# Optimization experiments

Measured on AMD Instinct MI355X. Metric: run time of the kernel, lower is better.

## Reference

```python
import jax, jax.numpy as jnp
import numpy as np
from jax import lax

B, T, H, W, C = 1, 8, 32, 32, 512


def _rmsnorm(x, gamma):
    # x / (||x||_2 + 1e-8) * sqrt(C) * gamma  (matches FlaxHunyuanVideo15RMSNorm)
    n = x / (jnp.linalg.norm(x, axis=-1, keepdims=True) + 1e-8)
    return n * (x.shape[-1] ** 0.5) * gamma


def _conv3d(x, w, b):
    # x: [B,T,H,W,Cin], w: [kt,kh,kw,Cin,Cout] (DHWIO), VALID padding
    y = lax.conv_general_dilated(x, w, (1, 1, 1), 'VALID',
                                 dimension_numbers=('NDHWC', 'DHWIO', 'NDHWC'))
    return y + b


def _causal_conv3d(x, w, b):
    # replicate pad: time (2,0) causal, spatial (1,1) each side, then valid 3x3x3 conv
    xp = jnp.pad(x, [(0, 0), (2, 0), (1, 1), (1, 1), (0, 0)], mode='edge')
    return _conv3d(xp, w, b)


def _conv1x1(x, w, b):
    # w: [1,1,1,Cin,Cout]
    return jnp.einsum('bthwc,cd->bthwd', x, w[0, 0, 0]) + b


def _resnet(x, g1, w1, b1, g2, w2, b2):
    h = jax.nn.silu(_rmsnorm(x, g1))
    h = _causal_conv3d(h, w1, b1)
    h = jax.nn.silu(_rmsnorm(h, g2))
    h = _causal_conv3d(h, w2, b2)
    return h + x


def _attn(x, g, qw, qb, kw, kb, vw, vb, pw, pb):
    identity = x
    xn = _rmsnorm(x, g)
    b, t, h, w, c = xn.shape
    n_hw = h * w
    s = t * n_hw
    q = _conv1x1(xn, qw, qb).reshape(b, s, c)
    k = _conv1x1(xn, kw, kb).reshape(b, s, c)
    v = _conv1x1(xn, vw, vb).reshape(b, s, c)
    # block-causal frame mask: query at frame f attends to keys with frame <= f
    fid = jnp.arange(s) // n_hw
    mask = jnp.where(fid[None, :] <= fid[:, None], 0.0, -jnp.inf).astype(q.dtype)
    scale = 1.0 / jnp.sqrt(jnp.asarray(c, q.dtype))
    scores = jnp.einsum('bqc,bkc->bqk', q, k) * scale + mask  # [B,S,S]
    attn = jax.nn.softmax(scores, axis=-1)
    o = jnp.einsum('bqk,bkc->bqc', attn, v).reshape(b, t, h, w, c)
    o = _conv1x1(o, pw, pb)
    return o + identity


def _forward(x, r1_g1, r1_w1, r1_b1, r1_g2, r1_w2, r1_b2,
             at_g, q_w, q_b, k_w, k_b, v_w, v_b, p_w, p_b,
             r2_g1, r2_w1, r2_b1, r2_g2, r2_w2, r2_b2):
    h = _resnet(x, r1_g1, r1_w1, r1_b1, r1_g2, r1_w2, r1_b2)
    h = _attn(h, at_g, q_w, q_b, k_w, k_b, v_w, v_b, p_w, p_b)
    h = _resnet(h, r2_g1, r2_w1, r2_b1, r2_g2, r2_w2, r2_b2)
    return h


def setup_inputs() -> dict:
    key = jax.random.key(0)
    ks = jax.random.split(key, 10)
    w3 = lambda k: jax.random.normal(k, (3, 3, 3, C, C), jnp.float32) * 0.02
    w1 = lambda k: jax.random.normal(k, (1, 1, 1, C, C), jnp.float32) * 0.02
    zc = jnp.zeros((C,), jnp.float32)
    oc = jnp.ones((C,), jnp.float32)
    return dict(
        x=jax.random.normal(ks[0], (B, T, H, W, C), jnp.float32),
        r1_g1=oc, r1_w1=w3(ks[1]), r1_b1=zc,
        r1_g2=oc, r1_w2=w3(ks[2]), r1_b2=zc,
        at_g=oc,
        q_w=w1(ks[3]), q_b=zc,
        k_w=w1(ks[4]), k_b=zc,
        v_w=w1(ks[5]), v_b=zc,
        p_w=w1(ks[6]), p_b=zc,
        r2_g1=oc, r2_w1=w3(ks[7]), r2_b1=zc,
        r2_g2=oc, r2_w2=w3(ks[8]), r2_b2=zc,
    )


def reference(x, r1_g1, r1_w1, r1_b1, r1_g2, r1_w2, r1_b2,
              at_g, q_w, q_b, k_w, k_b, v_w, v_b, p_w, p_b,
              r2_g1, r2_w1, r2_b1, r2_g2, r2_w2, r2_b2):
    return _forward(x, r1_g1, r1_w1, r1_b1, r1_g2, r1_w2, r1_b2,
                    at_g, q_w, q_b, k_w, k_b, v_w, v_b, p_w, p_b,
                    r2_g1, r2_w1, r2_b1, r2_g2, r2_w2, r2_b2)
```

## Files before the change

### kernel.cpp

```cpp
#include <hip/hip_runtime.h>
#include <cstdint>
#include <cstddef>

typedef __attribute__((ext_vector_type(4))) float floatx4;
typedef __attribute__((ext_vector_type(8))) short short8;

__device__ __forceinline__ short f2bf(float x) {
  union { float f; unsigned u; } c; c.f = x;
  unsigned r = (c.u + 0x7FFFu + ((c.u >> 16) & 1u)) >> 16;
  return (short)r;
}

__device__ __forceinline__ float bf2f(short x) {
  union { unsigned u; float f; } c; c.u = ((unsigned)(unsigned short)x) << 16;
  return c.f;
}

__device__ __forceinline__ floatx4 mfma16(short8 a, short8 b, floatx4 c) {
  return __builtin_amdgcn_mfma_f32_16x16x32_bf16(a, b, c, 0, 0, 0);
}

template <typename T>
__device__ __forceinline__ void gl_lds16(const T* g, T* l) {
  __builtin_amdgcn_global_load_lds(
      (__attribute__((address_space(1))) void*)g,
      (__attribute__((address_space(3))) void*)l, 16, 0, 0);
}

#define MEMFENCE asm volatile("" ::: "memory")
#define WAITV8 asm volatile("s_waitcnt vmcnt(8)" ::: "memory")

template <bool PAD, bool SILU>
__global__ __launch_bounds__(256) void norm_kernel(const float* __restrict__ src,
                                                   const float* __restrict__ gamma,
                                                   short* __restrict__ dst) {
  const int tid = threadIdx.x;
  const int wv = tid >> 6, lane = tid & 63;
  const int id = blockIdx.x * 4 + wv;
  int srow;
  if (PAD) {
    int tp = id / 1156, rem = id - tp * 1156;
    int hp = rem / 34, wp = rem - hp * 34;
    int t = tp - 2; t = t < 0 ? 0 : t;
    int h = hp - 1; h = h < 0 ? 0 : (h > 31 ? 31 : h);
    int w = wp - 1; w = w < 0 ? 0 : (w > 31 ? 31 : w);
    srow = (t << 10) + (h << 5) + w;
  } else {
    srow = id;
  }
  const float* sp = src + (size_t)srow * 512 + lane * 8;
  float4 v0 = *(const float4*)sp;
  float4 v1 = *(const float4*)(sp + 4);
  float a[8] = {v0.x, v0.y, v0.z, v0.w, v1.x, v1.y, v1.z, v1.w};
  float ss = 0.f;
#pragma unroll
  for (int i = 0; i < 8; ++i) ss += a[i] * a[i];
#pragma unroll
  for (int off = 32; off > 0; off >>= 1) ss += __shfl_xor(ss, off);
  const float scale = 22.627416997969522f / (sqrtf(ss) + 1e-8f);
  const float* gp = gamma + lane * 8;
  float4 g0 = *(const float4*)gp;
  float4 g1 = *(const float4*)(gp + 4);
  float g[8] = {g0.x, g0.y, g0.z, g0.w, g1.x, g1.y, g1.z, g1.w};
  short8 ov;
#pragma unroll
  for (int i = 0; i < 8; ++i) {
    float y = a[i] * scale * g[i];
    if (SILU) y = y / (1.f + __expf(-y));
    ov[i] = f2bf(y);
  }
  *(short8*)(dst + (size_t)id * 512 + lane * 8) = ov;
}

template <int NP>
__global__ __launch_bounds__(256) void combine_norm(const float* __restrict__ P0,
                                                    const float* __restrict__ P1,
                                                    const float* __restrict__ P2,
                                                    const float* __restrict__ bias,
                                                    const float* __restrict__ gamma,
                                                    short* __restrict__ dst) {
  const int tid = threadIdx.x;
  const int wv = tid >> 6, lane = tid & 63;
  const int id = blockIdx.x * 4 + wv;
  int tp = id / 1156, rem = id - tp * 1156;
  int hp = rem / 34, wp = rem - hp * 34;
  int t = tp - 2; t = t < 0 ? 0 : t;
  int h = hp - 1; h = h < 0 ? 0 : (h > 31 ? 31 : h);
  int w = wp - 1; w = w < 0 ? 0 : (w > 31 ? 31 : w);
  const size_t base = (size_t)((t << 10) + (h << 5) + w) * 512 + lane * 8;
  float a[8];
  {
    float4 a0 = *(const float4*)(P0 + base), a1 = *(const float4*)(P0 + base + 4);
    float4 b0 = *(const float4*)(P1 + base), b1 = *(const float4*)(P1 + base + 4);
    float4 z0 = *(const float4*)(bias + lane * 8), z1 = *(const float4*)(bias + lane * 8 + 4);
    a[0] = a0.x + b0.x + z0.x; a[1] = a0.y + b0.y + z0.y;
    a[2] = a0.z + b0.z + z0.z; a[3] = a0.w + b0.w + z0.w;
    a[4] = a1.x + b1.x + z1.x; a[5] = a1.y + b1.y + z1.y;
    a[6] = a1.z + b1.z + z1.z; a[7] = a1.w + b1.w + z1.w;
    if (NP == 3) {
      float4 c0 = *(const float4*)(P2 + base), c1 = *(const float4*)(P2 + base + 4);
      a[0] += c0.x; a[1] += c0.y; a[2] += c0.z; a[3] += c0.w;
      a[4] += c1.x; a[5] += c1.y; a[6] += c1.z; a[7] += c1.w;
    }
  }
  float ss = 0.f;
#pragma unroll
  for (int i = 0; i < 8; ++i) ss += a[i] * a[i];
#pragma unroll
  for (int off = 32; off > 0; off >>= 1) ss += __shfl_xor(ss, off);
  const float scale = 22.627416997969522f / (sqrtf(ss) + 1e-8f);
  float4 g0 = *(const float4*)(gamma + lane * 8), g1 = *(const float4*)(gamma + lane * 8 + 4);
  float g[8] = {g0.x, g0.y, g0.z, g0.w, g1.x, g1.y, g1.z, g1.w};
  short8 ov;
#pragma unroll
  for (int i = 0; i < 8; ++i) {
    float y = a[i] * scale * g[i];
    y = y / (1.f + __expf(-y));
    ov[i] = f2bf(y);
  }
  *(short8*)(dst + (size_t)id * 512 + lane * 8) = ov;
}

__global__ __launch_bounds__(256) void transpose_w(const float* __restrict__ src,
                                                   short* __restrict__ dst, int R, int C) {
  __shared__ float t[32][33];
  const int tx = threadIdx.x & 31, ty = threadIdx.x >> 5;
  const int r0 = (int)blockIdx.x << 5, c0 = (int)blockIdx.y << 5;
#pragma unroll
  for (int i = 0; i < 4; ++i)
    t[ty + i * 8][tx] = src[(size_t)(r0 + ty + i * 8) * C + c0 + tx];
  __syncthreads();
#pragma unroll
  for (int i = 0; i < 4; ++i)
    dst[(size_t)(c0 + ty + i * 8) * R + r0 + tx] = f2bf(t[tx][ty + i * 8]);
}

template <int NP>
__global__ __launch_bounds__(256) void conv_gemm_sp(const short* __restrict__ Xp,
                                                    const short* __restrict__ WT,
                                                    float* __restrict__ P0,
                                                    float* __restrict__ P1,
                                                    float* __restrict__ P2) {
  __shared__ __attribute__((aligned(16))) short Alds[2][4096];
  __shared__ __attribute__((aligned(16))) short Blds[2][4096];
  const int tid = threadIdx.x;
  const int wv = tid >> 6, lane = tid & 63;
  const int m0 = (int)blockIdx.x << 7, n0 = (int)blockIdx.y << 7;
  const int z = blockIdx.z;
  float* __restrict__ dst = (NP == 3) ? (z == 0 ? P0 : (z == 1 ? P1 : P2))
                                      : (z ? P1 : P0);

  const int swz = (((lane & 3) ^ ((lane >> 3) & 3)) << 3);
  int aoff[2], boff[2];
#pragma unroll
  for (int j = 0; j < 2; ++j) {
    const int chunk = wv * 2 + j;
    const int m = m0 + chunk * 16 + (lane >> 2);
    const int t = m >> 10, h = (m >> 5) & 31, w = m & 31;
    aoff[j] = (t * 1156 + h * 34 + w) * 512 + swz;
    const int n = n0 + chunk * 16 + (lane >> 2);
    boff[j] = n * 13824 + swz;
  }
  const int wm = (wv & 1) << 6, wn = (wv >> 1) << 6;
  floatx4 acc[4][4];
#pragma unroll
  for (int i = 0; i < 4; ++i)
#pragma unroll
    for (int j = 0; j < 4; ++j) acc[i][j] = 0.f;

  const int la = (lane & 15) * 32 + ((((lane >> 4) ^ ((lane >> 1) & 3))) << 3);
  const int span = 432 / NP;
  const int k0 = z * span, k1 = k0 + span;

  auto stage = [&](int kk, int buf) {
    const int tap = kk >> 4;
    const int cin0 = (kk & 15) << 5;
    const int dt = tap / 9;
    const int r9 = tap - dt * 9;
    const int dh = r9 / 3;
    const int dw = r9 - dh * 3;
    const int tapoff = (dt * 1156 + dh * 34 + dw) * 512 + cin0;
#pragma unroll
    for (int j = 0; j < 2; ++j) {
      const int chunk = wv * 2 + j;
      gl_lds16(Xp + aoff[j] + tapoff, &Alds[buf][chunk * 512]);
      gl_lds16(WT + boff[j] + (kk << 5), &Blds[buf][chunk * 512]);
    }
  };

  stage(k0, 0);
  for (int kk = k0; kk < k1; ++kk) {
    const int cur = (kk - k0) & 1;
    __syncthreads();
    if (kk + 1 < k1) stage(kk + 1, cur ^ 1);
    short8 af[4], bf[4];
#pragma unroll
    for (int i = 0; i < 4; ++i) af[i] = *(const short8*)&Alds[cur][(wm + i * 16) * 32 + la];
#pragma unroll
    for (int j = 0; j < 4; ++j) bf[j] = *(const short8*)&Blds[cur][(wn + j * 16) * 32 + la];
#pragma unroll
    for (int i = 0; i < 4; ++i)
#pragma unroll
      for (int j = 0; j < 4; ++j) acc[i][j] = mfma16(af[i], bf[j], acc[i][j]);
  }

  const int rbase = m0 + wm + (lane >> 4) * 4;
#pragma unroll
  for (int i = 0; i < 4; ++i) {
    const int row = rbase + i * 16;
#pragma unroll
    for (int j = 0; j < 4; ++j) {
      const int col = n0 + wn + j * 16 + (lane & 15);
#pragma unroll
      for (int r = 0; r < 4; ++r)
        dst[(size_t)(row + r) * 512 + col] = acc[i][j][r];
    }
  }
}

template <int NP, bool HAS_RES>
__global__ __launch_bounds__(256) void conv_combine(const float* __restrict__ P0,
                                                    const float* __restrict__ P1,
                                                    const float* __restrict__ P2,
                                                    const float* __restrict__ bias,
                                                    const float* __restrict__ res,
                                                    float* __restrict__ out) {
  const size_t i = ((size_t)blockIdx.x * 256 + threadIdx.x) * 4;
  float4 a = *(const float4*)(P0 + i);
  float4 b = *(const float4*)(P1 + i);
  float4 bz = *(const float4*)(bias + (int)(i & 511));
  float4 r;
  r.x = a.x + b.x + bz.x;
  r.y = a.y + b.y + bz.y;
  r.z = a.z + b.z + bz.z;
  r.w = a.w + b.w + bz.w;
  if (NP == 3) {
    float4 c = *(const float4*)(P2 + i);
    r.x += c.x; r.y += c.y; r.z += c.z; r.w += c.w;
  }
  if (HAS_RES) {
    float4 rs = *(const float4*)(res + i);
    r.x += rs.x; r.y += rs.y; r.z += rs.z; r.w += rs.w;
  }
  *(float4*)(out + i) = r;
}

template <int EPI>
__global__ __launch_bounds__(256) void gemm_bt(const short* __restrict__ A,
                                               const short* __restrict__ BT, int kdim,
                                               const float* __restrict__ b0,
                                               const float* __restrict__ b1,
                                               const float* __restrict__ b2,
                                               short* __restrict__ o0,
                                               short* __restrict__ o1,
                                               short* __restrict__ o2,
                                               float* oF, const float* res) {
  __shared__ __attribute__((aligned(16))) short Alds[2][4096];
  __shared__ __attribute__((aligned(16))) short Blds[2][4096];
  const int tid = threadIdx.x;
  const int wv = tid >> 6, lane = tid & 63;
  const int m0 = (int)blockIdx.x << 7, n0 = (int)blockIdx.y << 7;
  const int swz = (((lane & 3) ^ ((lane >> 3) & 3)) << 3);
  int aoff[2], boff[2];
#pragma unroll
  for (int j = 0; j < 2; ++j) {
    const int chunk = wv * 2 + j;
    aoff[j] = (m0 + chunk * 16 + (lane >> 2)) * kdim + swz;
    boff[j] = (n0 + chunk * 16 + (lane >> 2)) * kdim + swz;
  }
  const int wm = (wv & 1) << 6, wn = (wv >> 1) << 6;
  floatx4 acc[4][4];
#pragma unroll
  for (int i = 0; i < 4; ++i)
#pragma unroll
    for (int j = 0; j < 4; ++j) acc[i][j] = 0.f;
  const int la = (lane & 15) * 32 + ((((lane >> 4) ^ ((lane >> 1) & 3))) << 3);
  const int kiters = kdim >> 5;

  auto stage = [&](int kk, int buf) {
#pragma unroll
    for (int j = 0; j < 2; ++j) {
      const int chunk = wv * 2 + j;
      gl_lds16(A + aoff[j] + (kk << 5), &Alds[buf][chunk * 512]);
      gl_lds16(BT + boff[j] + (kk << 5), &Blds[buf][chunk * 512]);
    }
  };

  stage(0, 0);
  for (int kk = 0; kk < kiters; ++kk) {
    const int cur = kk & 1;
    __syncthreads();
    if (kk + 1 < kiters) stage(kk + 1, cur ^ 1);
    short8 af[4], bf[4];
#pragma unroll
    for (int i = 0; i < 4; ++i) af[i] = *(const short8*)&Alds[cur][(wm + i * 16) * 32 + la];
#pragma unroll
    for (int j = 0; j < 4; ++j) bf[j] = *(const short8*)&Blds[cur][(wn + j * 16) * 32 + la];
#pragma unroll
    for (int i = 0; i < 4; ++i)
#pragma unroll
      for (int j = 0; j < 4; ++j) acc[i][j] = mfma16(af[i], bf[j], acc[i][j]);
  }

  const int rbase = m0 + wm + (lane >> 4) * 4;
#pragma unroll
  for (int i = 0; i < 4; ++i) {
    const int row = rbase + i * 16;
#pragma unroll
    for (int j = 0; j < 4; ++j) {
      const int col = n0 + wn + j * 16 + (lane & 15);
      if (EPI == 0) {
        const int sel = col >> 9;
        const int c = col & 511;
        const float* bp = sel == 0 ? b0 : (sel == 1 ? b1 : b2);
        const float bz = bp[c];
#pragma unroll
        for (int r = 0; r < 4; ++r) {
          const int rr = row + r;
          const short v = f2bf(acc[i][j][r] + bz);
          if (sel == 0) {
            o0[(size_t)rr * 512 + c] = v;
          } else if (sel == 1) {
            o1[(size_t)(rr >> 5) * 16384 + ((c >> 5) << 10) + (((c >> 3) & 3) << 8) +
               ((rr & 31) << 3) + (c & 7)] = v;
          } else {
            o2[(size_t)(rr >> 5) * 16384 + (((rr >> 3) & 3) << 12) + (c << 3) + (rr & 7)] = v;
          }
        }
      } else {
        const float bz = b0[col];
#pragma unroll
        for (int r = 0; r < 4; ++r) {
          const size_t idx = (size_t)(row + r) * 512 + col;
          oF[idx] = acc[i][j][r] + bz + res[idx];
        }
      }
    }
  }
}

__global__ __launch_bounds__(256, 2) void attn_partial(const short* __restrict__ Q,
                                                       const short* __restrict__ Ksw,
                                                       const short* __restrict__ Vsw,
                                                       short* __restrict__ OpA,
                                                       short* __restrict__ OpB,
                                                       float* __restrict__ Lp) {
  __shared__ __attribute__((aligned(16))) short Klds[16384];
  __shared__ __attribute__((aligned(16))) short Vlds[16384];
  __shared__ __attribute__((aligned(16))) short Plds[4][512];
  const int tid = threadIdx.x;
  const int wv = tid >> 6, lane = tid & 63;
  const int cl = lane & 15, quad = lane >> 4;
  const int bid = (int)blockIdx.x;
  const int x8 = bid & 7, jj = bid >> 3;
  int y, qb;
  if (jj < 64) {
    y = x8 + ((jj >> 4) << 3);
    qb = jj & 15;
  } else {
    const int L = x8 * 8 + (jj - 64);
    y = 32 + (L >> 4);
    qb = L & 15;
  }
  int f = 0;
  while ((f + 1) * (f + 2) / 2 <= y) ++f;
  const int chunk = y - f * (f + 1) / 2;
  const int pidx = y * 16 + qb;
  const int q0 = (f << 10) + (qb << 6);

  short8 qf[16];
  {
    const short* qp = Q + (size_t)(q0 + wv * 16 + cl) * 512 + quad * 8;
#pragma unroll
    for (int kc = 0; kc < 16; ++kc) qf[kc] = *(const short8*)(qp + kc * 32);
  }
  floatx4 o[32];
#pragma unroll
  for (int i = 0; i < 32; ++i) o[i] = 0.f;
  float lr[4] = {0.f, 0.f, 0.f, 0.f};
  const float c1 = 0.063758716f;
  const short* klb = Klds + quad * 256 + cl * 8;
  const short* vlb = Vlds + quad * 4096 + cl * 8;
  const int swr = ((cl >> 1) & 3) << 3;

  auto stageK = [&](int kt) {
    const size_t tb = (size_t)((chunk << 5) + kt) * 16384;
#pragma unroll
    for (int j = 0; j < 8; ++j) {
      const int row = (j * 4 + wv) << 9;
      gl_lds16(Ksw + tb + row + lane * 8, &Klds[row]);
    }
  };
  auto stageV = [&](int kt) {
    const size_t tb = (size_t)((chunk << 5) + kt) * 16384;
#pragma unroll
    for (int j = 0; j < 8; ++j) {
      const int row = (j * 4 + wv) << 9;
      gl_lds16(Vsw + tb + row + lane * 8, &Vlds[row]);
    }
  };

  stageK(0);
  stageV(0);

  for (int kt = 0; kt < 32; ++kt) {
    WAITV8;
    __builtin_amdgcn_s_barrier();
    MEMFENCE;

    floatx4 s0 = 0.f, s1 = 0.f;
    __builtin_amdgcn_s_setprio(1);
#pragma unroll
    for (int kc = 0; kc < 16; ++kc) {
      short8 k0 = *(const short8*)(klb + kc * 1024);
      short8 k1 = *(const short8*)(klb + kc * 1024 + 128);
      s0 = mfma16(qf[kc], k0, s0);
      s1 = mfma16(qf[kc], k1, s1);
    }
    __builtin_amdgcn_s_setprio(0);

    MEMFENCE;
    __builtin_amdgcn_s_barrier();
    MEMFENCE;
    if (kt + 1 < 32) stageK(kt + 1);

#pragma unroll
    for (int r = 0; r < 4; ++r) {
      const float p0 = exp2f(s0[r] * c1), p1 = exp2f(s1[r] * c1);
      lr[r] += p0 + p1;
      const int qlr = quad * 4 + r;
      const int sw = ((qlr >> 1) & 3) << 3;
      const int oi = qlr * 32 + (cl ^ sw);
      Plds[wv][oi] = f2bf(p0);
      Plds[wv][oi ^ 16] = f2bf(p1);
    }

    WAITV8;
    __builtin_amdgcn_s_barrier();
    MEMFENCE;

    const short8 pf = *(const short8*)&Plds[wv][cl * 32 + ((quad << 3) ^ swr)];
    __builtin_amdgcn_s_setprio(1);
#pragma unroll
    for (int cn = 0; cn < 32; ++cn) {
      const short8 vf = *(const short8*)(vlb + cn * 128);
      o[cn] = mfma16(pf, vf, o[cn]);
    }
    __builtin_amdgcn_s_setprio(0);

    MEMFENCE;
    __builtin_amdgcn_s_barrier();
    MEMFENCE;
    if (kt + 1 < 32) stageV(kt + 1);
  }

#pragma unroll
  for (int r = 0; r < 4; ++r) {
    float v = lr[r];
    v += __shfl_xor(v, 1);
    v += __shfl_xor(v, 2);
    v += __shfl_xor(v, 4);
    v += __shfl_xor(v, 8);
    lr[r] = v;
  }

  short* base = pidx < 216 ? OpA + (size_t)pidx * 32768 : OpB + (size_t)(pidx - 216) * 32768;
  const int lrow0 = wv * 16 + quad * 4;
#pragma unroll
  for (int cn = 0; cn < 32; ++cn) {
    const int col = cn * 16 + cl;
#pragma unroll
    for (int r = 0; r < 4; ++r)
      base[(size_t)(lrow0 + r) * 512 + col] = f2bf(o[cn][r]);
  }
  if (cl == 0) {
#pragma unroll
    for (int r = 0; r < 4; ++r) Lp[pidx * 64 + lrow0 + r] = lr[r];
  }
}

__global__ __launch_bounds__(256) void attn_combine(const short* __restrict__ OpA,
                                                    const short* __restrict__ OpB,
                                                    const float* __restrict__ Lp,
                                                    short* __restrict__ O) {
  const int tid = threadIdx.x;
  const int wv = tid >> 6, lane = tid & 63;
  const int row = (int)blockIdx.x * 4 + wv;
  const int f = row >> 10, n = f + 1;
  const int qb = (row >> 6) & 15, lrow = row & 63;
  const int tri = f * (f + 1) / 2;
  float den = 0.f, acc[8];
#pragma unroll
  for (int i = 0; i < 8; ++i) acc[i] = 0.f;
#pragma unroll
  for (int ch = 0; ch < 8; ++ch) {
    if (ch < n) {
      const int pidx = (tri + ch) * 16 + qb;
      den += Lp[pidx * 64 + lrow];
      const short* b = pidx < 216 ? OpA + (size_t)pidx * 32768 : OpB + (size_t)(pidx - 216) * 32768;
      const short8 v = *(const short8*)(b + (size_t)lrow * 512 + lane * 8);
#pragma unroll
      for (int i = 0; i < 8; ++i) acc[i] += bf2f(v[i]);
    }
  }
  const float inv = 1.f / den;
  short8 ov;
#pragma unroll
  for (int i = 0; i < 8; ++i) ov[i] = f2bf(acc[i] * inv);
  *(short8*)(O + (size_t)row * 512 + lane * 8) = ov;
}

extern "C" void kernel_launch(void* const* d_in, const int* in_sizes, int n_in,
                              void* d_out, int out_size, void* d_ws, size_t ws_size,
                              hipStream_t stream) {
  const float* x     = (const float*)d_in[0];
  const float* r1_g1 = (const float*)d_in[1];
  const float* r1_w1 = (const float*)d_in[2];
  const float* r1_b1 = (const float*)d_in[3];
  const float* r1_g2 = (const float*)d_in[4];
  const float* r1_w2 = (const float*)d_in[5];
  const float* r1_b2 = (const float*)d_in[6];
  const float* at_g  = (const float*)d_in[7];
  const float* q_w   = (const float*)d_in[8];
  const float* q_b   = (const float*)d_in[9];
  const float* k_w   = (const float*)d_in[10];
  const float* k_b   = (const float*)d_in[11];
  const float* v_w   = (const float*)d_in[12];
  const float* v_b   = (const float*)d_in[13];
  const float* p_w   = (const float*)d_in[14];
  const float* p_b   = (const float*)d_in[15];
  const float* r2_g1 = (const float*)d_in[16];
  const float* r2_w1 = (const float*)d_in[17];
  const float* r2_b1 = (const float*)d_in[18];
  const float* r2_g2 = (const float*)d_in[19];
  const float* r2_w2 = (const float*)d_in[20];
  const float* r2_b2 = (const float*)d_in[21];
  float* out = (float*)d_out;

  char* ws = (char*)d_ws;
  size_t off = 0;
  auto alloc = [&](size_t bytes) -> void* {
    void* p = ws + off;
    off = (off + bytes + 255) & ~(size_t)255;
    return p;
  };
  short* wT    = (short*)alloc(27ull * 512 * 512 * 2);
  short* wqkvT = (short*)alloc(1536ull * 512 * 2);
  short* pwT   = (short*)alloc(512ull * 512 * 2);
  short* Xp    = (short*)alloc(10ull * 34 * 34 * 512 * 2);
  float* Y     = (float*)alloc(8192ull * 512 * 4);
  float* hA    = (float*)alloc(8192ull * 512 * 4);
  short* xn    = (short*)alloc(8192ull * 512 * 2);
  short* Qb    = (short*)alloc(8192ull * 512 * 2);
  short* Ksw   = (short*)alloc(8192ull * 512 * 2);
  short* Vsw   = (short*)alloc(8192ull * 512 * 2);
  float* Lp    = (float*)alloc(576ull * 64 * 4);
  (void)ws_size; (void)in_sizes; (void)n_in; (void)out_size;

  short* OpA = wT;
  short* OpB = Xp;
  float* P0  = (float*)xn;
  float* P1  = (float*)Ksw;
  float* P2  = Y;

  const dim3 b256(256);
  const dim3 convg3(64, 4, 3);
  const dim3 convg2(64, 4, 2);

  transpose_w<<<dim3(432, 16), b256, 0, stream>>>(r1_w1, wT, 13824, 512);
  norm_kernel<true, true><<<2890, b256, 0, stream>>>(x, r1_g1, Xp);
  conv_gemm_sp<3><<<convg3, b256, 0, stream>>>(Xp, wT, P0, P1, P2);
  transpose_w<<<dim3(432, 16), b256, 0, stream>>>(r1_w2, wT, 13824, 512);
  combine_norm<3><<<2890, b256, 0, stream>>>(P0, P1, P2, r1_b1, r1_g2, Xp);
  conv_gemm_sp<3><<<convg3, b256, 0, stream>>>(Xp, wT, P0, P1, P2);
  conv_combine<3, true><<<4096, b256, 0, stream>>>(P0, P1, P2, r1_b2, x, hA);

  norm_kernel<false, false><<<2048, b256, 0, stream>>>(hA, at_g, xn);
  transpose_w<<<dim3(16, 16), b256, 0, stream>>>(q_w, wqkvT, 512, 512);
  transpose_w<<<dim3(16, 16), b256, 0, stream>>>(k_w, wqkvT + 512 * 512, 512, 512);
  transpose_w<<<dim3(16, 16), b256, 0, stream>>>(v_w, wqkvT + 1024 * 512, 512, 512);
  transpose_w<<<dim3(16, 16), b256, 0, stream>>>(p_w, pwT, 512, 512);
  gemm_bt<0><<<dim3(64, 12), b256, 0, stream>>>(xn, wqkvT, 512, q_b, k_b, v_b,
                                                Qb, Ksw, Vsw, nullptr, nullptr);
  attn_partial<<<576, b256, 0, stream>>>(Qb, Ksw, Vsw, OpA, OpB, Lp);
  attn_combine<<<2048, b256, 0, stream>>>(OpA, OpB, Lp, xn);
  gemm_bt<1><<<dim3(64, 4), b256, 0, stream>>>(xn, pwT, 512, p_b, nullptr, nullptr,
                                               nullptr, nullptr, nullptr, hA, hA);

  transpose_w<<<dim3(432, 16), b256, 0, stream>>>(r2_w1, wT, 13824, 512);
  norm_kernel<true, true><<<2890, b256, 0, stream>>>(hA, r2_g1, Xp);
  conv_gemm_sp<2><<<convg2, b256, 0, stream>>>(Xp, wT, P0, P1, P2);
  transpose_w<<<dim3(432, 16), b256, 0, stream>>>(r2_w2, wT, 13824, 512);
  combine_norm<2><<<2890, b256, 0, stream>>>(P0, P1, P2, r2_b1, r2_g2, Xp);
  conv_gemm_sp<2><<<convg2, b256, 0, stream>>>(Xp, wT, P0, P1, P2);
  conv_combine<2, true><<<4096, b256, 0, stream>>>(P0, P1, P2, r2_b2, hA, out);
}
```

Before: 1.039 ms.

## Replace conv GEMM with 256x256-tile 8-wave kernel and uniform 4-way split-K

The causal conv implicit GEMM moves from 128x128 tiles with 4 waves and 3/2-way split-K to 256x256 tiles with 8 waves, 64-wide K steps and a fixed 4-way split-K. Global-to-LDS loads for the next stage are interleaved across four sub-phases with explicit vmcnt waits, barriers and setprio around the MFMA bursts. This aims to raise data reuse per LDS byte and overlap loads with compute. In exchange it needs much more LDS per block, fewer blocks, and an extra partial buffer (aliased to the output) to be summed in the combine kernels.

```diff
diff --git a/kernel.cpp b/kernel.cpp
--- a/kernel.cpp
+++ b/kernel.cpp
@@ -29,6 +29,8 @@
 
 #define MEMFENCE asm volatile("" ::: "memory")
 #define WAITV8 asm volatile("s_waitcnt vmcnt(8)" ::: "memory")
+#define WAITV2 asm volatile("s_waitcnt vmcnt(2)" ::: "memory")
+#define WAITV0 asm volatile("s_waitcnt vmcnt(0)" ::: "memory")
 
 template <bool PAD, bool SILU>
 __global__ __launch_bounds__(256) void norm_kernel(const float* __restrict__ src,
@@ -72,10 +74,10 @@
   *(short8*)(dst + (size_t)id * 512 + lane * 8) = ov;
 }
 
-template <int NP>
 __global__ __launch_bounds__(256) void combine_norm(const float* __restrict__ P0,
                                                     const float* __restrict__ P1,
                                                     const float* __restrict__ P2,
+                                                    const float* __restrict__ P3,
                                                     const float* __restrict__ bias,
                                                     const float* __restrict__ gamma,
                                                     short* __restrict__ dst) {
@@ -92,16 +94,17 @@
   {
     float4 a0 = *(const float4*)(P0 + base), a1 = *(const float4*)(P0 + base + 4);
     float4 b0 = *(const float4*)(P1 + base), b1 = *(const float4*)(P1 + base + 4);
+    float4 c0 = *(const float4*)(P2 + base), c1 = *(const float4*)(P2 + base + 4);
+    float4 d0 = *(const float4*)(P3 + base), d1 = *(const float4*)(P3 + base + 4);
     float4 z0 = *(const float4*)(bias + lane * 8), z1 = *(const float4*)(bias + lane * 8 + 4);
-    a[0] = a0.x + b0.x + z0.x; a[1] = a0.y + b0.y + z0.y;
-    a[2] = a0.z + b0.z + z0.z; a[3] = a0.w + b0.w + z0.w;
-    a[4] = a1.x + b1.x + z1.x; a[5] = a1.y + b1.y + z1.y;
-    a[6] = a1.z + b1.z + z1.z; a[7] = a1.w + b1.w + z1.w;
-    if (NP == 3) {
-      float4 c0 = *(const float4*)(P2 + base), c1 = *(const float4*)(P2 + base + 4);
-      a[0] += c0.x; a[1] += c0.y; a[2] += c0.z; a[3] += c0.w;
-      a[4] += c1.x; a[5] += c1.y; a[6] += c1.z; a[7] += c1.w;
-    }
+    a[0] = a0.x + b0.x + c0.x + d0.x + z0.x;
+    a[1] = a0.y + b0.y + c0.y + d0.y + z0.y;
+    a[2] = a0.z + b0.z + c0.z + d0.z + z0.z;
+    a[3] = a0.w + b0.w + c0.w + d0.w + z0.w;
+    a[4] = a1.x + b1.x + c1.x + d1.x + z1.x;
+    a[5] = a1.y + b1.y + c1.y + d1.y + z1.y;
+    a[6] = a1.z + b1.z + c1.z + d1.z + z1.z;
+    a[7] = a1.w + b1.w + c1.w + d1.w + z1.w;
   }
   float ss = 0.f;
 #pragma unroll
@@ -135,109 +138,163 @@
     dst[(size_t)(c0 + ty + i * 8) * R + r0 + tx] = f2bf(t[tx][ty + i * 8]);
 }
 
-template <int NP>
-__global__ __launch_bounds__(256) void conv_gemm_sp(const short* __restrict__ Xp,
-                                                    const short* __restrict__ WT,
-                                                    float* __restrict__ P0,
-                                                    float* __restrict__ P1,
-                                                    float* __restrict__ P2) {
-  __shared__ __attribute__((aligned(16))) short Alds[2][4096];
-  __shared__ __attribute__((aligned(16))) short Blds[2][4096];
+__global__ __launch_bounds__(512, 2) void conv_gemm8(const short* __restrict__ Xp,
+                                                     const short* __restrict__ WT,
+                                                     float* __restrict__ P0,
+                                                     float* __restrict__ P1,
+                                                     float* __restrict__ P2,
+                                                     float* __restrict__ P3) {
+  __shared__ __attribute__((aligned(16))) short Alds[2][16384];
+  __shared__ __attribute__((aligned(16))) short Blds[2][16384];
   const int tid = threadIdx.x;
-  const int wv = tid >> 6, lane = tid & 63;
-  const int m0 = (int)blockIdx.x << 7, n0 = (int)blockIdx.y << 7;
+  const int wid = tid >> 6, lane = tid & 63;
+  const int m0 = (int)blockIdx.x << 8, n0 = (int)blockIdx.y << 8;
   const int z = blockIdx.z;
-  float* __restrict__ dst = (NP == 3) ? (z == 0 ? P0 : (z == 1 ? P1 : P2))
-                                      : (z ? P1 : P0);
-
-  const int swz = (((lane & 3) ^ ((lane >> 3) & 3)) << 3);
-  int aoff[2], boff[2];
-#pragma unroll
-  for (int j = 0; j < 2; ++j) {
-    const int chunk = wv * 2 + j;
-    const int m = m0 + chunk * 16 + (lane >> 2);
+  float* __restrict__ dst = z == 0 ? P0 : (z == 1 ? P1 : (z == 2 ? P2 : P3));
+  const int wm = (wid >> 2) << 7, wn = (wid & 3) << 6;
+
+  const int logslot = (tid & 7) ^ ((tid >> 3) & 7);
+  int aoffA[4], boffB[4];
+#pragma unroll
+  for (int q = 0; q < 4; ++q) {
+    const int m = m0 + q * 64 + (tid >> 3);
     const int t = m >> 10, h = (m >> 5) & 31, w = m & 31;
-    aoff[j] = (t * 1156 + h * 34 + w) * 512 + swz;
-    const int n = n0 + chunk * 16 + (lane >> 2);
-    boff[j] = n * 13824 + swz;
-  }
-  const int wm = (wv & 1) << 6, wn = (wv >> 1) << 6;
-  floatx4 acc[4][4];
-#pragma unroll
-  for (int i = 0; i < 4; ++i)
-#pragma unroll
-    for (int j = 0; j < 4; ++j) acc[i][j] = 0.f;
-
-  const int la = (lane & 15) * 32 + ((((lane >> 4) ^ ((lane >> 1) & 3))) << 3);
-  const int span = 432 / NP;
-  const int k0 = z * span, k1 = k0 + span;
-
-  auto stage = [&](int kk, int buf) {
-    const int tap = kk >> 4;
-    const int cin0 = (kk & 15) << 5;
+    aoffA[q] = (t * 1156 + h * 34 + w) * 512 + logslot * 8;
+    boffB[q] = (n0 + q * 64 + (tid >> 3)) * 13824 + logslot * 8;
+  }
+  const int lwb = wid * 512;
+
+  const int frow = lane & 15;
+  const int fslot = lane >> 4;
+  const int sx = lane & 7;
+
+  floatx4 acc[4][2][4];
+#pragma unroll
+  for (int p = 0; p < 4; ++p)
+#pragma unroll
+    for (int i = 0; i < 2; ++i)
+#pragma unroll
+      for (int j = 0; j < 4; ++j) acc[p][i][j] = 0.f;
+
+  const int k0g = z * 54;
+
+  auto tapoff_of = [&](int kkg) {
+    const int tap = kkg >> 3;
     const int dt = tap / 9;
     const int r9 = tap - dt * 9;
     const int dh = r9 / 3;
     const int dw = r9 - dh * 3;
-    const int tapoff = (dt * 1156 + dh * 34 + dw) * 512 + cin0;
-#pragma unroll
-    for (int j = 0; j < 2; ++j) {
-      const int chunk = wv * 2 + j;
-      gl_lds16(Xp + aoff[j] + tapoff, &Alds[buf][chunk * 512]);
-      gl_lds16(WT + boff[j] + (kk << 5), &Blds[buf][chunk * 512]);
-    }
+    return (dt * 1156 + dh * 34 + dw) * 512 + ((kkg & 7) << 6);
   };
 
-  stage(k0, 0);
-  for (int kk = k0; kk < k1; ++kk) {
-    const int cur = (kk - k0) & 1;
-    __syncthreads();
-    if (kk + 1 < k1) stage(kk + 1, cur ^ 1);
-    short8 af[4], bf[4];
-#pragma unroll
-    for (int i = 0; i < 4; ++i) af[i] = *(const short8*)&Alds[cur][(wm + i * 16) * 32 + la];
-#pragma unroll
-    for (int j = 0; j < 4; ++j) bf[j] = *(const short8*)&Blds[cur][(wn + j * 16) * 32 + la];
-#pragma unroll
-    for (int i = 0; i < 4; ++i)
-#pragma unroll
-      for (int j = 0; j < 4; ++j) acc[i][j] = mfma16(af[i], bf[j], acc[i][j]);
-  }
-
-  const int rbase = m0 + wm + (lane >> 4) * 4;
-#pragma unroll
-  for (int i = 0; i < 4; ++i) {
-    const int row = rbase + i * 16;
-#pragma unroll
-    for (int j = 0; j < 4; ++j) {
-      const int col = n0 + wn + j * 16 + (lane & 15);
-#pragma unroll
-      for (int r = 0; r < 4; ++r)
-        dst[(size_t)(row + r) * 512 + col] = acc[i][j][r];
-    }
-  }
-}
-
-template <int NP, bool HAS_RES>
+  {
+    const int to = tapoff_of(k0g);
+#pragma unroll
+    for (int q = 0; q < 4; ++q) {
+      gl_lds16(Xp + aoffA[q] + to, &Alds[0][q * 4096 + lwb]);
+      gl_lds16(WT + boffB[q] + (k0g << 6), &Blds[0][q * 4096 + lwb]);
+    }
+  }
+
+  for (int kk = 0; kk < 54; ++kk) {
+    const int buf = kk & 1;
+    const bool nx = (kk + 1 < 54);
+    const int kng = k0g + kk + 1;
+    const int ton = nx ? tapoff_of(kng) : 0;
+    short8 bfr[4][2];
+#pragma unroll
+    for (int p = 0; p < 4; ++p) {
+      if (p == 0) {
+        if (nx) {
+          gl_lds16(Xp + aoffA[0] + ton, &Alds[buf ^ 1][lwb]);
+          gl_lds16(Xp + aoffA[1] + ton, &Alds[buf ^ 1][4096 + lwb]);
+          WAITV2;
+        } else {
+          WAITV0;
+        }
+      } else if (nx) {
+        if (p == 1) {
+          gl_lds16(Xp + aoffA[2] + ton, &Alds[buf ^ 1][8192 + lwb]);
+          gl_lds16(Xp + aoffA[3] + ton, &Alds[buf ^ 1][12288 + lwb]);
+        } else if (p == 2) {
+          gl_lds16(WT + boffB[0] + (kng << 6), &Blds[buf ^ 1][lwb]);
+          gl_lds16(WT + boffB[1] + (kng << 6), &Blds[buf ^ 1][4096 + lwb]);
+        } else {
+          gl_lds16(WT + boffB[2] + (kng << 6), &Blds[buf ^ 1][8192 + lwb]);
+          gl_lds16(WT + boffB[3] + (kng << 6), &Blds[buf ^ 1][12288 + lwb]);
+        }
+      }
+      MEMFENCE;
+      __builtin_amdgcn_s_barrier();
+      MEMFENCE;
+      if (p == 0) {
+#pragma unroll
+        for (int fj = 0; fj < 4; ++fj)
+#pragma unroll
+          for (int ks = 0; ks < 2; ++ks) {
+            const int row = wn + fj * 16 + frow;
+            bfr[fj][ks] =
+                *(const short8*)&Blds[buf][row * 64 + (((ks << 2) + fslot) ^ sx) * 8];
+          }
+      }
+      short8 afr[2][2];
+#pragma unroll
+      for (int fi = 0; fi < 2; ++fi)
+#pragma unroll
+        for (int ks = 0; ks < 2; ++ks) {
+          const int row = wm + p * 32 + fi * 16 + frow;
+          afr[fi][ks] =
+              *(const short8*)&Alds[buf][row * 64 + (((ks << 2) + fslot) ^ sx) * 8];
+        }
+      __builtin_amdgcn_s_setprio(1);
+#pragma unroll
+      for (int fi = 0; fi < 2; ++fi)
+#pragma unroll
+        for (int fj = 0; fj < 4; ++fj)
+#pragma unroll
+          for (int ks = 0; ks < 2; ++ks)
+            acc[p][fi][fj] = mfma16(afr[fi][ks], bfr[fj][ks], acc[p][fi][fj]);
+      __builtin_amdgcn_s_setprio(0);
+      MEMFENCE;
+      __builtin_amdgcn_s_barrier();
+      MEMFENCE;
+    }
+  }
+
+#pragma unroll
+  for (int p = 0; p < 4; ++p)
+#pragma unroll
+    for (int fi = 0; fi < 2; ++fi) {
+      const int rb = m0 + wm + p * 32 + fi * 16 + (lane >> 4) * 4;
+#pragma unroll
+      for (int fj = 0; fj < 4; ++fj) {
+        const int col = n0 + wn + fj * 16 + (lane & 15);
+#pragma unroll
+        for (int r = 0; r < 4; ++r)
+          dst[(size_t)(rb + r) * 512 + col] = acc[p][fi][fj][r];
+      }
+    }
+}
+
+template <bool HAS_RES>
 __global__ __launch_bounds__(256) void conv_combine(const float* __restrict__ P0,
                                                     const float* __restrict__ P1,
                                                     const float* __restrict__ P2,
+                                                    const float* __restrict__ P3,
                                                     const float* __restrict__ bias,
                                                     const float* __restrict__ res,
                                                     float* __restrict__ out) {
   const size_t i = ((size_t)blockIdx.x * 256 + threadIdx.x) * 4;
   float4 a = *(const float4*)(P0 + i);
   float4 b = *(const float4*)(P1 + i);
+  float4 c = *(const float4*)(P2 + i);
+  float4 d = *(const float4*)(P3 + i);
   float4 bz = *(const float4*)(bias + (int)(i & 511));
   float4 r;
-  r.x = a.x + b.x + bz.x;
-  r.y = a.y + b.y + bz.y;
-  r.z = a.z + b.z + bz.z;
-  r.w = a.w + b.w + bz.w;
-  if (NP == 3) {
-    float4 c = *(const float4*)(P2 + i);
-    r.x += c.x; r.y += c.y; r.z += c.z; r.w += c.w;
-  }
+  r.x = a.x + b.x + c.x + d.x + bz.x;
+  r.y = a.y + b.y + c.y + d.y + bz.y;
+  r.z = a.z + b.z + c.z + d.z + bz.z;
+  r.w = a.w + b.w + c.w + d.w + bz.w;
   if (HAS_RES) {
     float4 rs = *(const float4*)(res + i);
     r.x += rs.x; r.y += rs.y; r.z += rs.z; r.w += rs.w;
@@ -562,18 +619,19 @@
   float* P0  = (float*)xn;
   float* P1  = (float*)Ksw;
   float* P2  = Y;
+  float* P3  = out;
 
   const dim3 b256(256);
-  const dim3 convg3(64, 4, 3);
-  const dim3 convg2(64, 4, 2);
+  const dim3 b512(512);
+  const dim3 convg(32, 2, 4);
 
   transpose_w<<<dim3(432, 16), b256, 0, stream>>>(r1_w1, wT, 13824, 512);
   norm_kernel<true, true><<<2890, b256, 0, stream>>>(x, r1_g1, Xp);
-  conv_gemm_sp<3><<<convg3, b256, 0, stream>>>(Xp, wT, P0, P1, P2);
+  conv_gemm8<<<convg, b512, 0, stream>>>(Xp, wT, P0, P1, P2, P3);
   transpose_w<<<dim3(432, 16), b256, 0, stream>>>(r1_w2, wT, 13824, 512);
-  combine_norm<3><<<2890, b256, 0, stream>>>(P0, P1, P2, r1_b1, r1_g2, Xp);
-  conv_gemm_sp<3><<<convg3, b256, 0, stream>>>(Xp, wT, P0, P1, P2);
-  conv_combine<3, true><<<4096, b256, 0, stream>>>(P0, P1, P2, r1_b2, x, hA);
+  combine_norm<<<2890, b256, 0, stream>>>(P0, P1, P2, P3, r1_b1, r1_g2, Xp);
+  conv_gemm8<<<convg, b512, 0, stream>>>(Xp, wT, P0, P1, P2, P3);
+  conv_combine<true><<<4096, b256, 0, stream>>>(P0, P1, P2, P3, r1_b2, x, hA);
 
   norm_kernel<false, false><<<2048, b256, 0, stream>>>(hA, at_g, xn);
   transpose_w<<<dim3(16, 16), b256, 0, stream>>>(q_w, wqkvT, 512, 512);
@@ -589,9 +647,9 @@
 
   transpose_w<<<dim3(432, 16), b256, 0, stream>>>(r2_w1, wT, 13824, 512);
   norm_kernel<true, true><<<2890, b256, 0, stream>>>(hA, r2_g1, Xp);
-  conv_gemm_sp<2><<<convg2, b256, 0, stream>>>(Xp, wT, P0, P1, P2);
+  conv_gemm8<<<convg, b512, 0, stream>>>(Xp, wT, P0, P1, P2, P3);
   transpose_w<<<dim3(432, 16), b256, 0, stream>>>(r2_w2, wT, 13824, 512);
-  combine_norm<2><<<2890, b256, 0, stream>>>(P0, P1, P2, r2_b1, r2_g2, Xp);
-  conv_gemm_sp<2><<<convg2, b256, 0, stream>>>(Xp, wT, P0, P1, P2);
-  conv_combine<2, true><<<4096, b256, 0, stream>>>(P0, P1, P2, r2_b2, hA, out);
-}
+  combine_norm<<<2890, b256, 0, stream>>>(P0, P1, P2, P3, r2_b1, r2_g2, Xp);
+  conv_gemm8<<<convg, b512, 0, stream>>>(Xp, wT, P0, P1, P2, P3);
+  conv_combine<true><<<4096, b256, 0, stream>>>(P0, P1, P2, P3, r2_b2, hA, out);
+}
```

Measured after the change: 981.3 us. -5.6%, faster.
